# Kernel tuning notes

Hardware: AMD Instinct MI355X
Metric: run time of the kernel (lower is better)

The kernel has to match this reference:

```python
import jax, jax.numpy as jnp
import numpy as np

ALPHA = 1.0
EPS = 1e-6

NUM_CLASSES = 100000
FEAT_DIM = 256
BATCH = 8192


def setup_inputs() -> dict:
    key = jax.random.key(0)
    k1, k2 = jax.random.split(key)
    features = jax.random.normal(k1, (BATCH, FEAT_DIM), dtype=jnp.float32)
    target = jax.random.randint(k2, (BATCH,), 0, NUM_CLASSES, dtype=jnp.int64)
    # centers bank initialized to zeros as in the torch module
    centers = jnp.zeros((NUM_CLASSES, FEAT_DIM), dtype=jnp.float32)
    return {"features": features, "target": target, "centers": centers}


def reference(features, target, centers):
    # gather per-sample class centers: [B, D]
    centers_batch = centers[target]
    # MSE loss over all elements (nn.MSELoss default reduction='mean')
    diff = centers_batch - features  # [B, D]
    center_loss = jnp.mean(diff * diff)
    # per-class appearance counts, gathered back per sample
    counts = jax.ops.segment_sum(
        jnp.ones((target.shape[0],), dtype=jnp.float32), target,
        num_segments=NUM_CLASSES)  # [C]
    appear = counts[target]  # [B]
    # per-sample scaled update, scatter-added into the centers bank
    upd = ALPHA * diff / (appear + EPS)[:, None]  # [B, D]
    delta = jax.ops.segment_sum(upd, target, num_segments=NUM_CLASSES)  # [C, D]
    new_centers = centers - delta
    return center_loss, new_centers
```

## Files before the change

### kernel.cpp

```cpp
#include <hip/hip_runtime.h>

#define BATCH    8192
#define FEAT     256
#define NCLASS   100000
#define EPS_C    1e-6f

#define NC_ELEMS (NCLASS * FEAT)
#define NVEC     (NC_ELEMS / 4)
#define COPY_BLOCKS (NVEC / 256)

__global__ void build_kernel(const int* __restrict__ target,
                             int* __restrict__ head,
                             int* __restrict__ next) {
    int b = blockIdx.x * blockDim.x + threadIdx.x;
    if (b < BATCH) next[b] = atomicExch(&head[target[b]], b);
}

__global__ void copy_kernel(const float* __restrict__ centers,
                            float* __restrict__ out) {
    __shared__ float wtail[4];
    int t = threadIdx.x;
    int w = t >> 6;
    int l = t & 63;
    size_t i = (size_t)blockIdx.x * 256 + t;
    float4 c4 = ((const float4*)centers)[i];

    float pw = __shfl_up(c4.w, 1, 64);
    if (l == 63) wtail[w] = c4.w;
    __syncthreads();
    if (l == 0) {
        if (w > 0) {
            pw = wtail[w - 1];
        } else if (blockIdx.x > 0) {
            pw = centers[(size_t)blockIdx.x * 1024 - 1];
        } else {
            pw = 0.0f;
        }
    }
    float4 ov = {pw, c4.x, c4.y, c4.z};
    ((float4*)out)[i] = ov;

    if (blockIdx.x == COPY_BLOCKS - 1 && t == 255) out[NC_ELEMS] = c4.w;
}

__global__ void update_kernel(const float* __restrict__ centers,
                              const float* __restrict__ features,
                              const int* __restrict__ target,
                              const int* __restrict__ head,
                              const int* __restrict__ next,
                              float* __restrict__ partials,
                              float* __restrict__ out) {
    int wv = (blockIdx.x * blockDim.x + threadIdx.x) >> 6;
    int l  = threadIdx.x & 63;
    int r  = target[wv];
    if (head[r] != wv) return;

    const float4 c4 = ((const float4*)(centers + (size_t)r * FEAT))[l];
    float4 sumf = {0.f, 0.f, 0.f, 0.f};
    int n = 0;
    for (int s = wv; s != -1; s = next[s]) {
        float4 f4 = ((const float4*)(features + (size_t)s * FEAT))[l];
        sumf.x += f4.x; sumf.y += f4.y; sumf.z += f4.z; sumf.w += f4.w;
        float dx = c4.x - f4.x, dy = c4.y - f4.y;
        float dz = c4.z - f4.z, dw = c4.w - f4.w;
        float sq = dx*dx + dy*dy + dz*dz + dw*dw;
        #pragma unroll
        for (int off = 32; off > 0; off >>= 1) sq += __shfl_down(sq, off, 64);
        if (l == 0) partials[s] = sq;
        n++;
    }
    float nf  = (float)n;
    float inv = 1.0f / (nf + EPS_C);
    float nx = c4.x - (nf * c4.x - sumf.x) * inv;
    float ny = c4.y - (nf * c4.y - sumf.y) * inv;
    float nz = c4.z - (nf * c4.z - sumf.z) * inv;
    float nw = c4.w - (nf * c4.w - sumf.w) * inv;

    float* orow = out + 1 + (size_t)r * FEAT + 4 * l;
    orow[0] = nx; orow[1] = ny; orow[2] = nz; orow[3] = nw;
}

__global__ void finalize_kernel(const float* __restrict__ partials,
                                float* __restrict__ out0) {
    float s = 0.0f;
    for (int i = threadIdx.x; i < BATCH; i += 256) s += partials[i];
    #pragma unroll
    for (int off = 32; off > 0; off >>= 1) s += __shfl_down(s, off, 64);
    __shared__ float red[4];
    int wave = threadIdx.x >> 6;
    int lane = threadIdx.x & 63;
    if (lane == 0) red[wave] = s;
    __syncthreads();
    if (threadIdx.x == 0) {
        out0[0] = (red[0] + red[1] + red[2] + red[3]) / (float)(BATCH * FEAT);
    }
}

extern "C" void kernel_launch(void* const* d_in, const int* in_sizes, int n_in,
                              void* d_out, int out_size, void* d_ws, size_t ws_size,
                              hipStream_t stream) {
    const float* features = (const float*)d_in[0];
    const int*   target   = (const int*)d_in[1];
    const float* centers  = (const float*)d_in[2];
    float* out = (float*)d_out;

    int*   head     = (int*)d_ws;
    int*   next     = head + NCLASS;
    float* partials = (float*)(next + BATCH);

    hipMemsetAsync(head, 0xFF, NCLASS * sizeof(int), stream);
    build_kernel<<<(BATCH + 255) / 256, 256, 0, stream>>>(target, head, next);
    copy_kernel<<<COPY_BLOCKS, 256, 0, stream>>>(centers, out);
    update_kernel<<<BATCH / 4, 256, 0, stream>>>(centers, features, target,
                                                 head, next, partials, out);
    finalize_kernel<<<1, 256, 0, stream>>>(partials, out);
}
```

Before: 205.7 us.

## Reorder copy after update, skip touched rows, fuse finalize and memset

Replaces the memset and the multi-block build with a single 1024-thread block that clears head and builds the per-class linked lists. The bulk copy now runs after the update kernel, skips rows already written by the update, and folds the loss reduction into block 0. This drops a memset and a launch and avoids rewriting updated rows. The cost is a serial single-block build over 100k head entries and an extra head lookup per copied vector.

```diff
diff --git a/kernel.cpp b/kernel.cpp
--- a/kernel.cpp
+++ b/kernel.cpp
@@ -9,38 +9,14 @@
 #define NVEC     (NC_ELEMS / 4)
 #define COPY_BLOCKS (NVEC / 256)
 
-__global__ void build_kernel(const int* __restrict__ target,
-                             int* __restrict__ head,
-                             int* __restrict__ next) {
-    int b = blockIdx.x * blockDim.x + threadIdx.x;
-    if (b < BATCH) next[b] = atomicExch(&head[target[b]], b);
-}
-
-__global__ void copy_kernel(const float* __restrict__ centers,
-                            float* __restrict__ out) {
-    __shared__ float wtail[4];
+__global__ void build1_kernel(const int* __restrict__ target,
+                              int* __restrict__ head,
+                              int* __restrict__ next) {
     int t = threadIdx.x;
-    int w = t >> 6;
-    int l = t & 63;
-    size_t i = (size_t)blockIdx.x * 256 + t;
-    float4 c4 = ((const float4*)centers)[i];
-
-    float pw = __shfl_up(c4.w, 1, 64);
-    if (l == 63) wtail[w] = c4.w;
+    for (int c = t; c < NCLASS; c += 1024) head[c] = -1;
     __syncthreads();
-    if (l == 0) {
-        if (w > 0) {
-            pw = wtail[w - 1];
-        } else if (blockIdx.x > 0) {
-            pw = centers[(size_t)blockIdx.x * 1024 - 1];
-        } else {
-            pw = 0.0f;
-        }
-    }
-    float4 ov = {pw, c4.x, c4.y, c4.z};
-    ((float4*)out)[i] = ov;
-
-    if (blockIdx.x == COPY_BLOCKS - 1 && t == 255) out[NC_ELEMS] = c4.w;
+    for (int b = t; b < BATCH; b += 1024)
+        next[b] = atomicExch(&head[target[b]], b);
 }
 
 __global__ void update_kernel(const float* __restrict__ centers,
@@ -80,19 +56,49 @@
     orow[0] = nx; orow[1] = ny; orow[2] = nz; orow[3] = nw;
 }
 
-__global__ void finalize_kernel(const float* __restrict__ partials,
-                                float* __restrict__ out0) {
-    float s = 0.0f;
-    for (int i = threadIdx.x; i < BATCH; i += 256) s += partials[i];
-    #pragma unroll
-    for (int off = 32; off > 0; off >>= 1) s += __shfl_down(s, off, 64);
-    __shared__ float red[4];
-    int wave = threadIdx.x >> 6;
-    int lane = threadIdx.x & 63;
-    if (lane == 0) red[wave] = s;
-    __syncthreads();
-    if (threadIdx.x == 0) {
-        out0[0] = (red[0] + red[1] + red[2] + red[3]) / (float)(BATCH * FEAT);
+__global__ void copy_kernel(const float* __restrict__ centers,
+                            const int* __restrict__ head,
+                            const float* __restrict__ partials,
+                            float* __restrict__ out) {
+    int t = threadIdx.x;
+    int w = t >> 6;
+    int l = t & 63;
+    size_t i = (size_t)blockIdx.x * 256 + t;
+    int r = (int)(i >> 6);
+    float4 c4 = ((const float4*)centers)[i];
+    bool tr = (head[r] != -1);
+    float pw = __shfl_up(c4.w, 1, 64);
+
+    if (l == 0) {
+        bool tp = (r > 0) && (head[r - 1] != -1);
+        if (r > 0 && !tp) {
+            float e0 = centers[(size_t)r * FEAT - 1];
+            if (!tr) {
+                float4 ov = {e0, c4.x, c4.y, c4.z};
+                ((float4*)out)[i] = ov;
+            } else {
+                out[4 * i] = e0;
+            }
+        } else if (!tr) {
+            out[4 * i + 1] = c4.x; out[4 * i + 2] = c4.y; out[4 * i + 3] = c4.z;
+        }
+    } else if (!tr) {
+        float4 ov = {pw, c4.x, c4.y, c4.z};
+        ((float4*)out)[i] = ov;
+    }
+
+    if (blockIdx.x == COPY_BLOCKS - 1 && t == 255 && !tr) out[NC_ELEMS] = c4.w;
+
+    if (blockIdx.x == 0) {
+        float s = 0.0f;
+        for (int k = t; k < BATCH; k += 256) s += partials[k];
+        #pragma unroll
+        for (int off = 32; off > 0; off >>= 1) s += __shfl_down(s, off, 64);
+        __shared__ float red[4];
+        if (l == 0) red[w] = s;
+        __syncthreads();
+        if (t == 0)
+            out[0] = (red[0] + red[1] + red[2] + red[3]) / (float)(BATCH * FEAT);
     }
 }
 
@@ -108,10 +114,8 @@
     int*   next     = head + NCLASS;
     float* partials = (float*)(next + BATCH);
 
-    hipMemsetAsync(head, 0xFF, NCLASS * sizeof(int), stream);
-    build_kernel<<<(BATCH + 255) / 256, 256, 0, stream>>>(target, head, next);
-    copy_kernel<<<COPY_BLOCKS, 256, 0, stream>>>(centers, out);
+    build1_kernel<<<1, 1024, 0, stream>>>(target, head, next);
     update_kernel<<<BATCH / 4, 256, 0, stream>>>(centers, features, target,
                                                  head, next, partials, out);
-    finalize_kernel<<<1, 256, 0, stream>>>(partials, out);
+    copy_kernel<<<COPY_BLOCKS, 256, 0, stream>>>(centers, head, partials, out);
 }
```

New measurement: 215.0 us. 4.5% more time.

## Use unaligned vector loads and grid-stride chunks in the shifted centers copy

Applied to the files above, without the earlier changes.

The copy kernel replaces the shuffle-plus-shared-memory scheme for the one-float output shift with direct unaligned 16-byte loads from the source offset by one element. Each thread now moves four float4s per chunk inside a fixed 2048-block grid-stride loop, instead of one float4 per thread across about 25k blocks. The update kernel's four scalar stores become a single unaligned vector store. The aim is to drop the sync and shuffle overhead and cut block-launch count in this bandwidth-bound copy, at the cost of misaligned global loads.

```diff
diff --git a/kernel.cpp b/kernel.cpp
--- a/kernel.cpp
+++ b/kernel.cpp
@@ -1,13 +1,18 @@
 #include <hip/hip_runtime.h>
 
-#define BATCH    8192
-#define FEAT     256
-#define NCLASS   100000
-#define EPS_C    1e-6f
+#define BATCH   8192
+#define FEAT    256
+#define NCLASS  100000
+#define EPS_C   1e-6f
 
 #define NC_ELEMS (NCLASS * FEAT)
 #define NVEC     (NC_ELEMS / 4)
-#define COPY_BLOCKS (NVEC / 256)
+#define CHUNK    1024
+#define NCHUNK   (NVEC / CHUNK)
+#define COPY_GRID 2048
+
+typedef float float4a __attribute__((vector_size(16)));
+typedef float4a float4u __attribute__((aligned(4)));
 
 __global__ void build_kernel(const int* __restrict__ target,
                              int* __restrict__ head,
@@ -18,29 +23,26 @@
 
 __global__ void copy_kernel(const float* __restrict__ centers,
                             float* __restrict__ out) {
-    __shared__ float wtail[4];
     int t = threadIdx.x;
-    int w = t >> 6;
-    int l = t & 63;
-    size_t i = (size_t)blockIdx.x * 256 + t;
-    float4 c4 = ((const float4*)centers)[i];
-
-    float pw = __shfl_up(c4.w, 1, 64);
-    if (l == 63) wtail[w] = c4.w;
-    __syncthreads();
-    if (l == 0) {
-        if (w > 0) {
-            pw = wtail[w - 1];
-        } else if (blockIdx.x > 0) {
-            pw = centers[(size_t)blockIdx.x * 1024 - 1];
+    for (int chunk = blockIdx.x; chunk < NCHUNK; chunk += gridDim.x) {
+        size_t base = (size_t)chunk * CHUNK + t;
+        const float* s = centers + 4 * base - 1;
+        float4u v0, v1, v2, v3;
+        if (base != 0) {
+            v0 = *(const float4u*)s;
         } else {
-            pw = 0.0f;
+            v0 = (float4u){0.f, centers[0], centers[1], centers[2]};
         }
+        v1 = *(const float4u*)(s + 1024);
+        v2 = *(const float4u*)(s + 2048);
+        v3 = *(const float4u*)(s + 3072);
+        float* d = out + 4 * base;
+        *(float4a*)(d)        = v0;
+        *(float4a*)(d + 1024) = v1;
+        *(float4a*)(d + 2048) = v2;
+        *(float4a*)(d + 3072) = v3;
     }
-    float4 ov = {pw, c4.x, c4.y, c4.z};
-    ((float4*)out)[i] = ov;
-
-    if (blockIdx.x == COPY_BLOCKS - 1 && t == 255) out[NC_ELEMS] = c4.w;
+    if (blockIdx.x == 0 && t == 0) out[NC_ELEMS] = centers[NC_ELEMS - 1];
 }
 
 __global__ void update_kernel(const float* __restrict__ centers,
@@ -76,8 +78,7 @@
     float nz = c4.z - (nf * c4.z - sumf.z) * inv;
     float nw = c4.w - (nf * c4.w - sumf.w) * inv;
 
-    float* orow = out + 1 + (size_t)r * FEAT + 4 * l;
-    orow[0] = nx; orow[1] = ny; orow[2] = nz; orow[3] = nw;
+    *(float4u*)(out + 1 + (size_t)r * FEAT + 4 * l) = (float4u){nx, ny, nz, nw};
 }
 
 __global__ void finalize_kernel(const float* __restrict__ partials,
@@ -110,7 +111,7 @@
 
     hipMemsetAsync(head, 0xFF, NCLASS * sizeof(int), stream);
     build_kernel<<<(BATCH + 255) / 256, 256, 0, stream>>>(target, head, next);
-    copy_kernel<<<COPY_BLOCKS, 256, 0, stream>>>(centers, out);
+    copy_kernel<<<COPY_GRID, 256, 0, stream>>>(centers, out);
     update_kernel<<<BATCH / 4, 256, 0, stream>>>(centers, features, target,
                                                  head, next, partials, out);
     finalize_kernel<<<1, 256, 0, stream>>>(partials, out);
```

After: 210.2 us. 1.02x slower.
